# Optimization experiments

Measured on AMD Instinct MI355X. Metric: run time of the kernel, lower is better.

Reference implementation:

```python
import jax, jax.numpy as jnp
import numpy as np

N = 10000   # nodes
E = 80000   # edges
B = 2       # batch
T = 12      # time steps
F_IN = 64
F_OUT = 64


def setup_inputs() -> dict:
    key = jax.random.key(0)
    ks = jax.random.split(key, 8)
    x = jax.random.normal(ks[0], (B, N, T, F_IN), dtype=jnp.float32)
    src = jax.random.randint(ks[1], (E,), 0, N)
    dst = jax.random.randint(ks[2], (E,), 0, N)
    s = 1.0 / np.sqrt(F_IN)
    W_pool = jax.random.uniform(ks[3], (F_IN, F_IN), jnp.float32, -s, s)
    b_pool = jax.random.uniform(ks[4], (F_IN,), jnp.float32, -s, s)
    W_neigh = jax.random.uniform(ks[5], (F_OUT, F_IN), jnp.float32, -s, s)
    W_self = jax.random.uniform(ks[6], (F_OUT, F_IN), jnp.float32, -s, s)
    bias = jnp.zeros((F_OUT,), jnp.float32)
    return dict(x=x, src=src, dst=dst, W_pool=W_pool, b_pool=b_pool,
                W_neigh=W_neigh, W_self=W_self, bias=bias)


def reference(x, src, dst, W_pool, b_pool, W_neigh, W_self, bias):
    # x: (B, N, T, F) -> (N, B, T, F); node dim first as SAGEConv expects
    h = jnp.transpose(x, (1, 0, 2, 3))
    # pool aggregator: per-node MLP + relu (done on nodes, then gathered per edge
    # -- identical math to gather-then-MLP since the MLP is per-node/elementwise)
    msg = jax.nn.relu(jnp.einsum('nbtf,gf->nbtg', h, W_pool) + b_pool)  # (N,B,T,F)
    m = msg[src]                                                        # (E,B,T,F) gather
    neigh = jax.ops.segment_max(m, dst, num_segments=N)                 # max-pool per dst node
    # zero-in-degree nodes get -inf from segment_max -> replace with 0 (DGL behavior)
    neigh = jnp.where(jnp.isfinite(neigh), neigh, jnp.zeros((), neigh.dtype))
    rst = (jnp.einsum('nbtf,of->nbto', h, W_self)
           + jnp.einsum('nbtf,of->nbto', neigh, W_neigh)
           + bias)                                                      # (N,B,T,F_OUT)
    return jnp.transpose(rst, (1, 0, 2, 3))                              # (B,N,T,F_OUT)
```

## Files before the change

### kernel.cpp

```cpp
#include <hip/hip_runtime.h>

#define NN 10000
#define NE 80000
#define NB 2
#define NT 12
#define NF 64
#define ROWS (NB*NN*NT)

typedef __attribute__((ext_vector_type(8))) short bf16x8;
typedef __attribute__((ext_vector_type(2))) unsigned short u16x2;
typedef __attribute__((ext_vector_type(4))) float f32x4;
typedef __attribute__((ext_vector_type(4))) float fv4;
typedef __attribute__((ext_vector_type(4))) unsigned int u32x4;
typedef __attribute__((ext_vector_type(2))) unsigned int u32x2;

#define QCLAMP 4.0f
#define QSCALE 63.75f

__device__ __forceinline__ unsigned short f2b(float f) {
    unsigned int u = __builtin_bit_cast(unsigned int, f);
    u += 0x7fffu + ((u >> 16) & 1u);
    return (unsigned short)(u >> 16);
}
__device__ __forceinline__ unsigned pmax16(unsigned a, unsigned b) {
    u16x2 x = __builtin_bit_cast(u16x2, a), y = __builtin_bit_cast(u16x2, b);
    return __builtin_bit_cast(unsigned, __builtin_elementwise_max(x, y));
}

__global__ __launch_bounds__(256) void k_msg(const float* __restrict__ x,
        const float* __restrict__ Wp, const float* __restrict__ bp,
        const int* __restrict__ dst, int* __restrict__ cnt,
        unsigned char* __restrict__ msg8, unsigned short* __restrict__ xb) {
    __shared__ __align__(16) unsigned short A[128*72];
    __shared__ __align__(16) unsigned short W[64*72];
    int tid = threadIdx.x;
    {
        int e = blockIdx.x * 256 + tid;
        if (e < NE) atomicAdd(&cnt[dst[e]], 1);
    }
    {
        int row = tid >> 2, c = (tid & 3) * 16;
        unsigned short ws16[16];
        #pragma unroll
        for (int i = 0; i < 4; ++i) {
            fv4 v = *(const fv4*)(Wp + row*64 + c + i*4);
            ws16[i*4+0] = f2b(v.x); ws16[i*4+1] = f2b(v.y);
            ws16[i*4+2] = f2b(v.z); ws16[i*4+3] = f2b(v.w);
        }
        *(bf16x8*)(W + row*72 + c)     = *(bf16x8*)&ws16[0];
        *(bf16x8*)(W + row*72 + c + 8) = *(bf16x8*)&ws16[8];
    }
    int m0 = blockIdx.x * 128;
    #pragma unroll
    for (int k = 0; k < 8; ++k) {
        int c = tid + 256*k;
        int row = c >> 4, f0 = (c & 15) * 4;
        int grow = m0 + row;
        fv4 v = __builtin_nontemporal_load((const fv4*)(x + (size_t)grow*64 + f0));
        uint2 p;
        p.x = f2b(v.x) | ((unsigned int)f2b(v.y) << 16);
        p.y = f2b(v.z) | ((unsigned int)f2b(v.w) << 16);
        *(uint2*)(A + row*72 + f0) = p;
        int b = grow / (NN*NT);
        int rem = grow - b*(NN*NT);
        int node = rem / NT, t = rem - node*NT;
        *(uint2*)(xb + ((size_t)node*24 + b*12 + t)*64 + f0) = p;
    }
    __syncthreads();

    int lane = tid & 63, w = tid >> 6;
    int cl = lane & 15, gq = lane >> 4;
    f32x4 acc[2][4] = {};
    #pragma unroll
    for (int kk = 0; kk < 2; ++kk) {
        int ko = kk*32 + gq*8;
        bf16x8 a0 = *(const bf16x8*)(A + (w*32 + cl)*72 + ko);
        bf16x8 a1 = *(const bf16x8*)(A + (w*32 + 16 + cl)*72 + ko);
        #pragma unroll
        for (int nf = 0; nf < 4; ++nf) {
            bf16x8 b = *(const bf16x8*)(W + (nf*16 + cl)*72 + ko);
            acc[0][nf] = __builtin_amdgcn_mfma_f32_16x16x32_bf16(a0, b, acc[0][nf], 0,0,0);
            acc[1][nf] = __builtin_amdgcn_mfma_f32_16x16x32_bf16(a1, b, acc[1][nf], 0,0,0);
        }
    }
    float bpv[4];
    #pragma unroll
    for (int nf = 0; nf < 4; ++nf) bpv[nf] = bp[nf*16 + cl];
    #pragma unroll
    for (int m = 0; m < 2; ++m)
    #pragma unroll
    for (int r = 0; r < 4; ++r) {
        int row = m0 + w*32 + m*16 + gq*4 + r;
        int b  = row / (NN*NT);
        int rem = row - b*(NN*NT);
        int node = rem / NT, t = rem - node*NT;
        unsigned q0 = (unsigned)(fminf(fmaxf(acc[m][0][r] + bpv[0], 0.f), QCLAMP)*QSCALE + 0.5f);
        unsigned q1 = (unsigned)(fminf(fmaxf(acc[m][1][r] + bpv[1], 0.f), QCLAMP)*QSCALE + 0.5f);
        unsigned q2 = (unsigned)(fminf(fmaxf(acc[m][2][r] + bpv[2], 0.f), QCLAMP)*QSCALE + 0.5f);
        unsigned q3 = (unsigned)(fminf(fmaxf(acc[m][3][r] + bpv[3], 0.f), QCLAMP)*QSCALE + 0.5f);
        *(unsigned*)(msg8 + ((size_t)(node*24 + b*12 + t) << 6) + cl*4) =
            q0 | (q1 << 8) | (q2 << 16) | (q3 << 24);
    }
}

__global__ __launch_bounds__(1024) void k_scan(const int* __restrict__ cnt,
        int* __restrict__ rowptr, int* __restrict__ wofs,
        const float* __restrict__ Wn, const float* __restrict__ Ws,
        unsigned short* __restrict__ Wcat) {
    int tid = threadIdx.x;
    for (int i = tid; i < 4096; i += 1024) {
        int o = i >> 6, g = i & 63;
        Wcat[o*128 + g] = f2b(Ws[i]);
        Wcat[o*128 + 64 + ((g & 15)*4 + (g >> 4))] = f2b(Wn[i] * (1.0f / QSCALE));
    }
    __shared__ int s[1024];
    const int C = 10;
    int base = tid * C;
    int loc[C];
    int sum = 0;
    for (int i = 0; i < C; ++i) {
        int idx = base + i;
        int v = (idx < NN) ? cnt[idx] : 0;
        loc[i] = sum;
        sum += v;
    }
    s[tid] = sum;
    __syncthreads();
    for (int off = 1; off < 1024; off <<= 1) {
        int v = (tid >= off) ? s[tid - off] : 0;
        __syncthreads();
        s[tid] += v;
        __syncthreads();
    }
    int prev = (tid == 0) ? 0 : s[tid - 1];
    for (int i = 0; i < C; ++i) {
        int idx = base + i;
        if (idx < NN) {
            int v = prev + loc[i];
            rowptr[idx] = v;
            wofs[idx]   = v;
        }
    }
    if (tid == 1023) rowptr[NN] = s[1023];
}

__global__ void k_scatter(const int* __restrict__ src, const int* __restrict__ dst,
        int* __restrict__ wofs, int* __restrict__ csr) {
    int e = blockIdx.x * blockDim.x + threadIdx.x;
    if (e < NE) {
        int pos = atomicAdd(&wofs[dst[e]], 1);
        csr[pos] = src[e];
    }
}

__global__ __launch_bounds__(256, 4) void k_out(const unsigned short* __restrict__ xb,
        const unsigned char* __restrict__ msg8, const unsigned short* __restrict__ Wcat,
        const float* __restrict__ bias,
        const int* __restrict__ rowptr, const int* __restrict__ csr,
        float* __restrict__ out) {
    __shared__ __align__(16) unsigned short NL[4*24*72 + 8*72];
    __shared__ __align__(16) float OT[4*24*64];
    int tid = threadIdx.x;
    int w = tid >> 6, lane = tid & 63;
    int n = blockIdx.x * 4 + w;
    unsigned short* tile = NL + w * (24*72);
    float* ot = OT + w * 1536;
    int cl = lane & 15, gq = lane >> 4;

    const unsigned short* xrow = xb + (size_t)n * 1536;
    bf16x8 a_self[2][2];
    #pragma unroll
    for (int kk = 0; kk < 2; ++kk) {
        int ko = kk*32 + gq*8;
        a_self[0][kk] = *(const bf16x8*)(xrow + cl*64 + ko);
        a_self[1][kk] = *(const bf16x8*)(xrow + (16 + cl)*64 + ko);
    }

    int rp0 = rowptr[n], rp1 = rowptr[n + 1];
    unsigned ae[6] = {0,0,0,0,0,0}, ao[6] = {0,0,0,0,0,0};
    #define ACC1(v, d) { ae[d] = pmax16(ae[d], (v) & 0x00FF00FFu); \
                         ao[d] = pmax16(ao[d], ((v) >> 8) & 0x00FF00FFu); }
    #define ACCE(a, b) { ACC1(a.x,0) ACC1(a.y,1) ACC1(a.z,2) ACC1(a.w,3) \
                         ACC1(b.x,4) ACC1(b.y,5) }
    int e = rp0;
    for (; e + 4 <= rp1; e += 4) {
        const unsigned char* p0 = msg8 + (size_t)csr[e  ]*1536;
        const unsigned char* p1 = msg8 + (size_t)csr[e+1]*1536;
        const unsigned char* p2 = msg8 + (size_t)csr[e+2]*1536;
        const unsigned char* p3 = msg8 + (size_t)csr[e+3]*1536;
        u32x4 A0 = __builtin_nontemporal_load((const u32x4*)(p0 + lane*16));
        u32x4 A1 = __builtin_nontemporal_load((const u32x4*)(p1 + lane*16));
        u32x4 A2 = __builtin_nontemporal_load((const u32x4*)(p2 + lane*16));
        u32x4 A3 = __builtin_nontemporal_load((const u32x4*)(p3 + lane*16));
        u32x2 B0 = __builtin_nontemporal_load((const u32x2*)(p0 + 1024 + lane*8));
        u32x2 B1 = __builtin_nontemporal_load((const u32x2*)(p1 + 1024 + lane*8));
        u32x2 B2 = __builtin_nontemporal_load((const u32x2*)(p2 + 1024 + lane*8));
        u32x2 B3 = __builtin_nontemporal_load((const u32x2*)(p3 + 1024 + lane*8));
        ACCE(A0, B0) ACCE(A1, B1) ACCE(A2, B2) ACCE(A3, B3)
    }
    for (; e < rp1; ++e) {
        const unsigned char* p0 = msg8 + (size_t)csr[e]*1536;
        u32x4 A0 = __builtin_nontemporal_load((const u32x4*)(p0 + lane*16));
        u32x2 B0 = __builtin_nontemporal_load((const u32x2*)(p0 + 1024 + lane*8));
        ACCE(A0, B0)
    }
    {
        unsigned short t16[16];
        #pragma unroll
        for (int d = 0; d < 4; ++d) {
            t16[4*d+0] = f2b((float)(ae[d] & 0xFFu));
            t16[4*d+1] = f2b((float)(ao[d] & 0xFFu));
            t16[4*d+2] = f2b((float)(ae[d] >> 16));
            t16[4*d+3] = f2b((float)(ao[d] >> 16));
        }
        *(bf16x8*)(tile + (lane>>2)*72 + (lane&3)*16)     = *(bf16x8*)&t16[0];
        *(bf16x8*)(tile + (lane>>2)*72 + (lane&3)*16 + 8) = *(bf16x8*)&t16[8];
        unsigned short t8[8];
        #pragma unroll
        for (int d = 4; d < 6; ++d) {
            t8[4*(d-4)+0] = f2b((float)(ae[d] & 0xFFu));
            t8[4*(d-4)+1] = f2b((float)(ao[d] & 0xFFu));
            t8[4*(d-4)+2] = f2b((float)(ae[d] >> 16));
            t8[4*(d-4)+3] = f2b((float)(ao[d] >> 16));
        }
        *(bf16x8*)(tile + (16 + (lane>>3))*72 + (lane&7)*8) = *(bf16x8*)&t8[0];
    }

    f32x4 acc0[4] = {}, acc1[4] = {};
    #pragma unroll
    for (int kk = 0; kk < 4; ++kk) {
        bf16x8 a0, a1;
        if (kk < 2) { a0 = a_self[0][kk]; a1 = a_self[1][kk]; }
        else {
            int ko = (kk - 2)*32 + gq*8;
            a0 = *(const bf16x8*)(tile + cl*72 + ko);
            a1 = *(const bf16x8*)(tile + (16 + cl)*72 + ko);
        }
        #pragma unroll
        for (int cg = 0; cg < 4; ++cg) {
            bf16x8 b = *(const bf16x8*)(Wcat + (cg*16 + cl)*128 + kk*32 + gq*8);
            acc0[cg] = __builtin_amdgcn_mfma_f32_16x16x32_bf16(a0, b, acc0[cg], 0,0,0);
            acc1[cg] = __builtin_amdgcn_mfma_f32_16x16x32_bf16(a1, b, acc1[cg], 0,0,0);
        }
    }
    #pragma unroll
    for (int cg = 0; cg < 4; ++cg) {
        float bv = bias[cg*16 + cl];
        #pragma unroll
        for (int r = 0; r < 4; ++r)
            ot[(gq*4 + r)*64 + cg*16 + cl] = acc0[cg][r] + bv;
        if (gq < 2) {
            #pragma unroll
            for (int r = 0; r < 4; ++r)
                ot[(16 + gq*4 + r)*64 + cg*16 + cl] = acc1[cg][r] + bv;
        }
    }
    #pragma unroll
    for (int b0 = 0; b0 < 2; ++b0) {
        float* og = out + (size_t)(b0*NN + n) * 768;
        #pragma unroll
        for (int j = 0; j < 3; ++j) {
            fv4 v = *(const fv4*)(ot + b0*768 + j*256 + lane*4);
            __builtin_nontemporal_store(v, (fv4*)(og + j*256 + lane*4));
        }
    }
}

extern "C" void kernel_launch(void* const* d_in, const int* in_sizes, int n_in,
                              void* d_out, int out_size, void* d_ws, size_t ws_size,
                              hipStream_t stream) {
    const float* x    = (const float*)d_in[0];
    const int*   src  = (const int*)  d_in[1];
    const int*   dst  = (const int*)  d_in[2];
    const float* Wp   = (const float*)d_in[3];
    const float* bp   = (const float*)d_in[4];
    const float* Wn   = (const float*)d_in[5];
    const float* Wsf  = (const float*)d_in[6];
    const float* bias = (const float*)d_in[7];
    float* out = (float*)d_out;

    char* ws = (char*)d_ws;
    int*            cnt    = (int*)           (ws);
    int*            rowptr = (int*)           (ws + 40064);
    int*            wofs   = (int*)           (ws + 80128);
    int*            csr    = (int*)           (ws + 120192);
    unsigned short* Wcat   = (unsigned short*)(ws + 448512);
    unsigned short* xb     = (unsigned short*)(ws + 464896);
    unsigned char*  msg8   = (unsigned char*) (ws + 31184896);

    hipMemsetAsync(cnt, 0, NN * sizeof(int), stream);
    k_msg    <<<ROWS/128, 256, 0, stream>>>(x, Wp, bp, dst, cnt, msg8, xb);
    k_scan   <<<1, 1024, 0, stream>>>(cnt, rowptr, wofs, Wn, Wsf, Wcat);
    k_scatter<<<(NE + 255) / 256, 256, 0, stream>>>(src, dst, wofs, csr);
    k_out    <<<NN/4, 256, 0, stream>>>(xb, msg8, Wcat, bias, rowptr, csr, out);
}
```

Before: 105.4 us.

## Split gather-max into sliced aggregation kernel with cache-friendly message layout

Lays out the quantized message tensor as 8 slices of 3 time rows each (about 1.9 MB per slice), so each slice can stay resident in L2 while a separate k_agg kernel does the per-slice neighbor max gather. The aggregated maxima go to a new nmax8 buffer, and the GEMM kernel just reads that row instead of gathering over edges. This swaps scattered 1.5 KB row gathers over the full 15 MB message array for slice-local gathers meant to hit cache. The cost is an extra kernel launch and an extra write and read of the aggregated buffer.

```diff
diff --git a/kernel.cpp b/kernel.cpp
--- a/kernel.cpp
+++ b/kernel.cpp
@@ -6,6 +6,7 @@
 #define NT 12
 #define NF 64
 #define ROWS (NB*NN*NT)
+#define SLICE_BYTES 1920000
 
 typedef __attribute__((ext_vector_type(8))) short bf16x8;
 typedef __attribute__((ext_vector_type(2))) unsigned short u16x2;
@@ -16,6 +17,7 @@
 
 #define QCLAMP 4.0f
 #define QSCALE 63.75f
+#define MEVEN 0x00FF00FFu
 
 __device__ __forceinline__ unsigned short f2b(float f) {
     unsigned int u = __builtin_bit_cast(unsigned int, f);
@@ -98,7 +100,8 @@
         unsigned q1 = (unsigned)(fminf(fmaxf(acc[m][1][r] + bpv[1], 0.f), QCLAMP)*QSCALE + 0.5f);
         unsigned q2 = (unsigned)(fminf(fmaxf(acc[m][2][r] + bpv[2], 0.f), QCLAMP)*QSCALE + 0.5f);
         unsigned q3 = (unsigned)(fminf(fmaxf(acc[m][3][r] + bpv[3], 0.f), QCLAMP)*QSCALE + 0.5f);
-        *(unsigned*)(msg8 + ((size_t)(node*24 + b*12 + t) << 6) + cl*4) =
+        int rr = b*12 + t, s = rr / 3;
+        *(unsigned*)(msg8 + (size_t)s*SLICE_BYTES + node*192 + (rr - s*3)*64 + cl*4) =
             q0 | (q1 << 8) | (q2 << 16) | (q3 << 24);
     }
 }
@@ -153,11 +156,45 @@
     }
 }
 
-__global__ __launch_bounds__(256, 4) void k_out(const unsigned short* __restrict__ xb,
-        const unsigned char* __restrict__ msg8, const unsigned short* __restrict__ Wcat,
-        const float* __restrict__ bias,
+__global__ __launch_bounds__(256, 8) void k_agg(const unsigned char* __restrict__ msg8,
         const int* __restrict__ rowptr, const int* __restrict__ csr,
-        float* __restrict__ out) {
+        unsigned char* __restrict__ nmax8) {
+    int s = blockIdx.x & 7;
+    int chunk = blockIdx.x >> 3;
+    int w = threadIdx.x >> 6, lane = threadIdx.x & 63;
+    int l48 = (lane < 48) ? lane : lane - 16;
+    int loff = l48 * 4;
+    const unsigned char* sb = msg8 + (size_t)s * SLICE_BYTES;
+    #pragma unroll 1
+    for (int i = 0; i < 8; ++i) {
+        int n = chunk*32 + w*8 + i;
+        if (n >= NN) break;
+        int rp0 = rowptr[n], rp1 = rowptr[n+1];
+        unsigned ae = 0, ao = 0;
+        int e = rp0;
+        for (; e + 4 <= rp1; e += 4) {
+            unsigned v0 = *(const unsigned*)(sb + (size_t)csr[e  ]*192 + loff);
+            unsigned v1 = *(const unsigned*)(sb + (size_t)csr[e+1]*192 + loff);
+            unsigned v2 = *(const unsigned*)(sb + (size_t)csr[e+2]*192 + loff);
+            unsigned v3 = *(const unsigned*)(sb + (size_t)csr[e+3]*192 + loff);
+            ae = pmax16(ae, pmax16(pmax16(v0 & MEVEN, v1 & MEVEN),
+                                   pmax16(v2 & MEVEN, v3 & MEVEN)));
+            ao = pmax16(ao, pmax16(pmax16((v0 >> 8) & MEVEN, (v1 >> 8) & MEVEN),
+                                   pmax16((v2 >> 8) & MEVEN, (v3 >> 8) & MEVEN)));
+        }
+        for (; e < rp1; ++e) {
+            unsigned v0 = *(const unsigned*)(sb + (size_t)csr[e]*192 + loff);
+            ae = pmax16(ae, v0 & MEVEN);
+            ao = pmax16(ao, (v0 >> 8) & MEVEN);
+        }
+        if (lane < 48)
+            *(unsigned*)(nmax8 + (size_t)n*1536 + s*192 + lane*4) = ae | (ao << 8);
+    }
+}
+
+__global__ __launch_bounds__(256, 4) void k_gemm(const unsigned short* __restrict__ xb,
+        const unsigned char* __restrict__ nmax8, const unsigned short* __restrict__ Wcat,
+        const float* __restrict__ bias, float* __restrict__ out) {
     __shared__ __align__(16) unsigned short NL[4*24*72 + 8*72];
     __shared__ __align__(16) float OT[4*24*64];
     int tid = threadIdx.x;
@@ -175,35 +212,13 @@
         a_self[0][kk] = *(const bf16x8*)(xrow + cl*64 + ko);
         a_self[1][kk] = *(const bf16x8*)(xrow + (16 + cl)*64 + ko);
     }
-
-    int rp0 = rowptr[n], rp1 = rowptr[n + 1];
-    unsigned ae[6] = {0,0,0,0,0,0}, ao[6] = {0,0,0,0,0,0};
-    #define ACC1(v, d) { ae[d] = pmax16(ae[d], (v) & 0x00FF00FFu); \
-                         ao[d] = pmax16(ao[d], ((v) >> 8) & 0x00FF00FFu); }
-    #define ACCE(a, b) { ACC1(a.x,0) ACC1(a.y,1) ACC1(a.z,2) ACC1(a.w,3) \
-                         ACC1(b.x,4) ACC1(b.y,5) }
-    int e = rp0;
-    for (; e + 4 <= rp1; e += 4) {
-        const unsigned char* p0 = msg8 + (size_t)csr[e  ]*1536;
-        const unsigned char* p1 = msg8 + (size_t)csr[e+1]*1536;
-        const unsigned char* p2 = msg8 + (size_t)csr[e+2]*1536;
-        const unsigned char* p3 = msg8 + (size_t)csr[e+3]*1536;
-        u32x4 A0 = __builtin_nontemporal_load((const u32x4*)(p0 + lane*16));
-        u32x4 A1 = __builtin_nontemporal_load((const u32x4*)(p1 + lane*16));
-        u32x4 A2 = __builtin_nontemporal_load((const u32x4*)(p2 + lane*16));
-        u32x4 A3 = __builtin_nontemporal_load((const u32x4*)(p3 + lane*16));
-        u32x2 B0 = __builtin_nontemporal_load((const u32x2*)(p0 + 1024 + lane*8));
-        u32x2 B1 = __builtin_nontemporal_load((const u32x2*)(p1 + 1024 + lane*8));
-        u32x2 B2 = __builtin_nontemporal_load((const u32x2*)(p2 + 1024 + lane*8));
-        u32x2 B3 = __builtin_nontemporal_load((const u32x2*)(p3 + 1024 + lane*8));
-        ACCE(A0, B0) ACCE(A1, B1) ACCE(A2, B2) ACCE(A3, B3)
-    }
-    for (; e < rp1; ++e) {
-        const unsigned char* p0 = msg8 + (size_t)csr[e]*1536;
-        u32x4 A0 = __builtin_nontemporal_load((const u32x4*)(p0 + lane*16));
-        u32x2 B0 = __builtin_nontemporal_load((const u32x2*)(p0 + 1024 + lane*8));
-        ACCE(A0, B0)
-    }
+    const unsigned char* nr = nmax8 + (size_t)n * 1536;
+    u32x4 A0 = *(const u32x4*)(nr + lane*16);
+    u32x2 B0 = *(const u32x2*)(nr + 1024 + lane*8);
+    unsigned ae[6], ao[6];
+    ae[0]=A0.x&MEVEN; ao[0]=(A0.x>>8)&MEVEN; ae[1]=A0.y&MEVEN; ao[1]=(A0.y>>8)&MEVEN;
+    ae[2]=A0.z&MEVEN; ao[2]=(A0.z>>8)&MEVEN; ae[3]=A0.w&MEVEN; ao[3]=(A0.w>>8)&MEVEN;
+    ae[4]=B0.x&MEVEN; ao[4]=(B0.x>>8)&MEVEN; ae[5]=B0.y&MEVEN; ao[5]=(B0.y>>8)&MEVEN;
     {
         unsigned short t16[16];
         #pragma unroll
@@ -287,10 +302,12 @@
     unsigned short* Wcat   = (unsigned short*)(ws + 448512);
     unsigned short* xb     = (unsigned short*)(ws + 464896);
     unsigned char*  msg8   = (unsigned char*) (ws + 31184896);
+    unsigned char*  nmax8  = (unsigned char*) (ws + 46544896);
 
     hipMemsetAsync(cnt, 0, NN * sizeof(int), stream);
     k_msg    <<<ROWS/128, 256, 0, stream>>>(x, Wp, bp, dst, cnt, msg8, xb);
     k_scan   <<<1, 1024, 0, stream>>>(cnt, rowptr, wofs, Wn, Wsf, Wcat);
     k_scatter<<<(NE + 255) / 256, 256, 0, stream>>>(src, dst, wofs, csr);
-    k_out    <<<NN/4, 256, 0, stream>>>(xb, msg8, Wcat, bias, rowptr, csr, out);
-}
+    k_agg    <<<((NN + 31) / 32) * 8, 256, 0, stream>>>(msg8, rowptr, csr, nmax8);
+    k_gemm   <<<NN/4, 256, 0, stream>>>(xb, nmax8, Wcat, bias, out);
+}
```

Result: slower. 114.8 us (+8.9%).
